# Kernel tuning notes

Measured on AMD Instinct MI355X. Metric: run time of the kernel, lower is better.

The kernel has to match this reference:

```python
import jax, jax.numpy as jnp
import numpy as np

B = 4096
D0, D1 = 256, 64


def setup_inputs() -> dict:
    key = jax.random.key(0)
    k0, k1, k2, k3 = jax.random.split(key, 4)
    return {
        "s0": jax.random.normal(k0, (B, D0), dtype=jnp.float32),
        "s1": jax.random.normal(k1, (B, D1), dtype=jnp.float32),
        "t0": jax.random.normal(k2, (B, D0), dtype=jnp.float32),
        "t1": jax.random.normal(k3, (B, D1), dtype=jnp.float32),
    }


def _gaussian_kernel(source, target):
    # feats: [2B, D]
    feats = jnp.concatenate([source, target], axis=0)
    n = feats.shape[0]
    # pairwise squared distances [2B, 2B] via the Gram-matrix identity
    # (same math as ((x - y) ** 2).sum(-1), avoids the [N, N, D] intermediate)
    sq = jnp.sum(feats * feats, axis=-1)
    dist = sq[:, None] + sq[None, :] - 2.0 * (feats @ feats.T)
    # median-heuristic bandwidth with num_kernels=1: gamma = (n^2 - n) / sum(dist)
    gamma = (n * n - n) / jnp.sum(jax.lax.stop_gradient(dist))
    return jnp.exp(-dist * gamma)


def reference(s0, s1, t0, t1):
    # joint kernel: elementwise product of per-stream Gaussian kernels
    k = _gaussian_kernel(s0, t0) * _gaussian_kernel(s1, t1)
    b = s0.shape[0]
    s2s = k[:b, :b]
    t2t = k[b:, b:]
    s2t = k[:b, b:]
    return jnp.mean(s2s + t2t - 2.0 * s2t)
```

## Files before the change

kernel.cpp:

```cpp
#include <hip/hip_runtime.h>
#include <hip/hip_fp8.h>

#define B_ROWS 4096
#define NTOT   8192
#define D0     256
#define D1     64
#define KDIM   320
#define NSB    128
#define NTILE  64
#define NTRI   2080

typedef __attribute__((ext_vector_type(4))) float f32x4;
typedef __attribute__((ext_vector_type(2))) long long2v;

#define OFF_GAM   0
#define OFF_PQ0   32
#define OFF_PQ1   544
#define OFF_P0    1056
#define OFF_P1    132128
#define OFF_R     164896
#define OFF_BSUM  197664
#define OFF_PHI   214304

__device__ __forceinline__ void load_lds16(const void* g, void* l) {
    __builtin_amdgcn_global_load_lds(
        (const __attribute__((address_space(1))) void*)g,
        (__attribute__((address_space(3))) void*)l, 16, 0, 0);
}

__global__ __launch_bounds__(256) void k_stats(
    const float* __restrict__ s0, const float* __restrict__ s1,
    const float* __restrict__ t0, const float* __restrict__ t1,
    float* __restrict__ part0, float* __restrict__ part1,
    float* __restrict__ pq0, float* __restrict__ pq1) {
    __shared__ float sh0[4][256];
    __shared__ float sh1[4][64];
    __shared__ float shq[4][2];
    int t = threadIdx.x, wv = t >> 6, lane = t & 63;
    int rb = blockIdx.x * 64;
    int c4 = lane * 4;
    int rr = wv;

    f32x4 cs = {0.f, 0.f, 0.f, 0.f};
    float q0 = 0.f;
    #pragma unroll 4
    for (int k = 0; k < 16; ++k) {
        int row = rb + rr + k * 4;
        const float* b0 = (row < B_ROWS) ? s0 + (size_t)row * D0 : t0 + (size_t)(row - B_ROWS) * D0;
        f32x4 v = *(const f32x4*)(b0 + c4);
        cs.x += v.x; cs.y += v.y; cs.z += v.z; cs.w += v.w;
        q0 += v.x * v.x + v.y * v.y + v.z * v.z + v.w * v.w;
    }
    *(f32x4*)&sh0[rr][c4] = cs;

    float cs1 = 0.f, q1 = 0.f;
    #pragma unroll 4
    for (int k = 0; k < 16; ++k) {
        int row = rb + rr + k * 4;
        const float* b1 = (row < B_ROWS) ? s1 + (size_t)row * D1 : t1 + (size_t)(row - B_ROWS) * D1;
        float v = b1[lane];
        cs1 += v; q1 += v * v;
    }
    sh1[rr][lane] = cs1;

    #pragma unroll
    for (int o = 32; o; o >>= 1) { q0 += __shfl_xor(q0, o, 64); q1 += __shfl_xor(q1, o, 64); }
    if (lane == 0) { shq[wv][0] = q0; shq[wv][1] = q1; }
    __syncthreads();

    part0[blockIdx.x * D0 + t] = sh0[0][t] + sh0[1][t] + sh0[2][t] + sh0[3][t];
    if (t < D1) part1[blockIdx.x * D1 + t] = sh1[0][t] + sh1[1][t] + sh1[2][t] + sh1[3][t];
    if (t == 0) {
        pq0[blockIdx.x] = shq[0][0] + shq[1][0] + shq[2][0] + shq[3][0];
        pq1[blockIdx.x] = shq[0][1] + shq[1][1] + shq[2][1] + shq[3][1];
    }
}

__global__ __launch_bounds__(256) void k_gamma(
    const float* __restrict__ pq0, const float* __restrict__ pq1,
    const float* __restrict__ part0, const float* __restrict__ part1,
    float* __restrict__ gam) {
    __shared__ double sh[4][4];
    int t = threadIdx.x, wv = t >> 6, lane = t & 63;

    double a0 = 0.0, a1 = 0.0;
    if (t < NSB) { a0 = (double)pq0[t]; a1 = (double)pq1[t]; }

    double F0t = 0.0;
    for (int b = 0; b < NSB; ++b) F0t += (double)part0[b * D0 + t];
    double nf0 = F0t * F0t;

    double nf1 = 0.0;
    if (t < D1) {
        double F1t = 0.0;
        for (int b = 0; b < NSB; ++b) F1t += (double)part1[b * D1 + t];
        nf1 = F1t * F1t;
    }

    #pragma unroll
    for (int o = 32; o; o >>= 1) {
        a0  += __shfl_xor(a0, o, 64);
        a1  += __shfl_xor(a1, o, 64);
        nf0 += __shfl_xor(nf0, o, 64);
        nf1 += __shfl_xor(nf1, o, 64);
    }
    if (lane == 0) { sh[wv][0] = a0; sh[wv][1] = a1; sh[wv][2] = nf0; sh[wv][3] = nf1; }
    __syncthreads();
    if (t == 0) {
        double b0 = 0, b1 = 0, b2 = 0, b3 = 0;
        for (int w = 0; w < 4; ++w) { b0 += sh[w][0]; b1 += sh[w][1]; b2 += sh[w][2]; b3 += sh[w][3]; }
        double n = (double)NTOT;
        double g0 = (n * n - n) / (2.0 * n * b0 - 2.0 * b2);
        double g1 = (n * n - n) / (2.0 * n * b1 - 2.0 * b3);
        gam[0] = (float)g0; gam[1] = (float)g1;
        gam[2] = (float)sqrt(g0); gam[3] = (float)sqrt(g1);
    }
}

__global__ __launch_bounds__(256) void k_pack(
    const float* __restrict__ s0, const float* __restrict__ s1,
    const float* __restrict__ t0, const float* __restrict__ t1,
    const float* __restrict__ gam, unsigned char* __restrict__ phi,
    float* __restrict__ rvec) {
    int wv = threadIdx.x >> 6, lane = threadIdx.x & 63;
    int row = blockIdx.x * 4 + wv;
    float sg0 = gam[2], sg1 = gam[3];
    const float* b0 = (row < B_ROWS) ? s0 + (size_t)row * D0 : t0 + (size_t)(row - B_ROWS) * D0;
    const float* b1 = (row < B_ROWS) ? s1 + (size_t)row * D1 : t1 + (size_t)(row - B_ROWS) * D1;
    unsigned char* pr = phi + (size_t)row * KDIM;
    f32x4 v = *(const f32x4*)(b0 + lane * 4);
    __hip_fp8_e4m3 q0(v.x * sg0), q1(v.y * sg0), q2(v.z * sg0), q3(v.w * sg0);
    unsigned int word = (unsigned int)q0.__x | ((unsigned int)q1.__x << 8) |
                        ((unsigned int)q2.__x << 16) | ((unsigned int)q3.__x << 24);
    int doff0 = ((lane >> 4) << 6) + (((lane >> 1) & 3) << 4) +
                (((lane >> 3) & 1) << 3) + ((lane & 1) << 2);
    *(unsigned int*)(pr + doff0) = word;
    float f0 = (float)q0, f1 = (float)q1, f2 = (float)q2, f3 = (float)q3;
    float p = f0 * f0 + f1 * f1 + f2 * f2 + f3 * f3;
    __hip_fp8_e4m3 qd(b1[lane] * sg1);
    int doff1 = 256 + (((lane >> 3) & 3) << 4) + (((lane >> 5) & 1) << 3) + (lane & 7);
    pr[doff1] = qd.__x;
    float fd = (float)qd;
    p += fd * fd;
    #pragma unroll
    for (int o = 32; o; o >>= 1) p += __shfl_xor(p, o, 64);
    if (lane == 0) rvec[row] = p;
}

__global__ __launch_bounds__(256, 3) void k_mmd(
    const unsigned char* __restrict__ phi, const float* __restrict__ rvec,
    double* __restrict__ blocksum) {
    int tb = blockIdx.x;
    int I = (int)((129.0f - sqrtf(16641.0f - 8.0f * (float)tb)) * 0.5f);
    while ((129 * I - I * I) / 2 > tb) --I;
    while ((129 * (I + 1) - (I + 1) * (I + 1)) / 2 <= tb) ++I;
    int J = I + (tb - (129 * I - I * I) / 2);

    __shared__ unsigned char As[24576];
    __shared__ unsigned char Bs[24576];
    __shared__ float rIl[128], rJl[128];
    __shared__ float wsum[4];

    int tid = threadIdx.x, wv = tid >> 6, lane = tid & 63;
    int wr = wv >> 1, wc = wv & 1;
    int rgrp = lane >> 4, rlow = lane & 15;
    const int rowA = I * 128, rowB = J * 128;

    if (tid < 128) rIl[tid] = rvec[rowA + tid];
    else           rJl[tid - 128] = rvec[rowB + (tid - 128)];

    f32x4 acc_[4][4] = {};

    #define STAGE(tbase, nt)                                                    \
        _Pragma("unroll")                                                       \
        for (int it = 0; it < (nt) * 2; ++it) {                                 \
            int idx = it * 256 + tid;                                           \
            int tt = idx >> 9, rs = idx & 511;                                  \
            int row = rs >> 2, slot = rs & 3;                                   \
            int rg = slot ^ ((row >> 1) & 3);                                   \
            size_t gcol = ((tbase) + tt) * 64 + rg * 16;                        \
            load_lds16(phi + (size_t)(rowA + row) * KDIM + gcol,                \
                       As + it * 4096 + wv * 1024);                             \
            load_lds16(phi + (size_t)(rowB + row) * KDIM + gcol,                \
                       Bs + it * 4096 + wv * 1024);                             \
        }

    #define COMPUTE(kkbase, nt)                                                 \
        _Pragma("unroll")                                                       \
        for (int tt = 0; tt < (nt); ++tt) {                                     \
            long2v af[4], bf[4];                                                \
            _Pragma("unroll")                                                   \
            for (int m = 0; m < 4; ++m) {                                       \
                int row = wr * 64 + m * 16 + rlow;                              \
                int slot = rgrp ^ ((row >> 1) & 3);                             \
                af[m] = *(const long2v*)&As[tt * 8192 + row * 64 + slot * 16];  \
            }                                                                   \
            _Pragma("unroll")                                                   \
            for (int n = 0; n < 4; ++n) {                                       \
                int col = wc * 64 + n * 16 + rlow;                              \
                int slot = rgrp ^ ((col >> 1) & 3);                             \
                bf[n] = *(const long2v*)&Bs[tt * 8192 + col * 64 + slot * 16];  \
            }                                                                   \
            _Pragma("unroll")                                                   \
            for (int m = 0; m < 4; ++m)                                         \
                _Pragma("unroll")                                               \
                for (int n = 0; n < 4; ++n) {                                   \
                    acc_[m][n] = __builtin_amdgcn_mfma_f32_16x16x32_fp8_fp8(    \
                        af[m][0], bf[n][0], acc_[m][n], 0, 0, 0);               \
                    acc_[m][n] = __builtin_amdgcn_mfma_f32_16x16x32_fp8_fp8(    \
                        af[m][1], bf[n][1], acc_[m][n], 0, 0, 0);               \
                }                                                               \
        }

    STAGE(0, 3);
    __syncthreads();
    COMPUTE(0, 3);
    __syncthreads();
    STAGE(3, 2);
    __syncthreads();
    COMPUTE(6, 2);

    float psum = 0.f;
    #pragma unroll
    for (int m = 0; m < 4; ++m) {
        float ri[4];
        #pragma unroll
        for (int j = 0; j < 4; ++j) ri[j] = rIl[wr * 64 + m * 16 + rgrp * 4 + j];
        #pragma unroll
        for (int n = 0; n < 4; ++n) {
            float rj = rJl[wc * 64 + n * 16 + rlow];
            f32x4 a = acc_[m][n];
            psum += __expf(2.f * a.x - ri[0] - rj);
            psum += __expf(2.f * a.y - ri[1] - rj);
            psum += __expf(2.f * a.z - ri[2] - rj);
            psum += __expf(2.f * a.w - ri[3] - rj);
        }
    }
    #pragma unroll
    for (int o = 32; o; o >>= 1) psum += __shfl_xor(psum, o, 64);
    if (lane == 0) wsum[wv] = psum;
    __syncthreads();
    if (tid == 0) {
        float bs = wsum[0] + wsum[1] + wsum[2] + wsum[3];
        double sgn = ((I < 32) == (J < 32)) ? 1.0 : -1.0;
        double fac = (I == J) ? 1.0 : 2.0;
        blocksum[tb] = sgn * fac * (double)bs;
    }
}

__global__ __launch_bounds__(256) void k_final(
    const double* __restrict__ blocksum, float* __restrict__ out) {
    __shared__ double sh[4];
    int t = threadIdx.x, wv = t >> 6, lane = t & 63;
    double s = 0.0;
    for (int i = t; i < NTRI; i += 256) s += blocksum[i];
    #pragma unroll
    for (int o = 32; o; o >>= 1) s += __shfl_xor(s, o, 64);
    if (lane == 0) sh[wv] = s;
    __syncthreads();
    if (t == 0) {
        double tot = sh[0] + sh[1] + sh[2] + sh[3];
        out[0] = (float)(tot / ((double)B_ROWS * (double)B_ROWS));
    }
}

extern "C" void kernel_launch(void* const* d_in, const int* in_sizes, int n_in,
                              void* d_out, int out_size, void* d_ws, size_t ws_size,
                              hipStream_t stream) {
    const float* s0 = (const float*)d_in[0];
    const float* s1 = (const float*)d_in[1];
    const float* t0 = (const float*)d_in[2];
    const float* t1 = (const float*)d_in[3];
    char* ws = (char*)d_ws;
    float*  gam  = (float*)(ws + OFF_GAM);
    float*  pq0  = (float*)(ws + OFF_PQ0);
    float*  pq1  = (float*)(ws + OFF_PQ1);
    float*  p0   = (float*)(ws + OFF_P0);
    float*  p1   = (float*)(ws + OFF_P1);
    float*  rvec = (float*)(ws + OFF_R);
    double* bsum = (double*)(ws + OFF_BSUM);
    unsigned char* phi = (unsigned char*)(ws + OFF_PHI);

    k_stats<<<NSB, 256, 0, stream>>>(s0, s1, t0, t1, p0, p1, pq0, pq1);
    k_gamma<<<1, 256, 0, stream>>>(pq0, pq1, p0, p1, gam);
    k_pack<<<2048, 256, 0, stream>>>(s0, s1, t0, t1, gam, phi, rvec);
    k_mmd<<<NTRI, 256, 0, stream>>>(phi, rvec, bsum);
    k_final<<<1, 256, 0, stream>>>(bsum, (float*)d_out);
}
```

Before: 49.73 us.

## Make MMD kernel persistent and prefetch next tile during exp epilogue

The MMD kernel now launches 768 persistent blocks, and each one strides over the 2080 triangular tiles. While the exp/reduction epilogue of the current tile runs, the block issues the async LDS loads for the first K-stage of its next tile. MFMA sections are also wrapped in s_setprio raises. The aim is to hide global-to-LDS latency and cut launch/tail overhead. The cost is that work is spread unevenly: 2080 tiles over 768 blocks gives 2 or 3 tiles per block, which can leave a tail imbalance.

```diff
diff --git a/kernel.cpp b/kernel.cpp
--- a/kernel.cpp
+++ b/kernel.cpp
@@ -9,6 +9,7 @@
 #define NSB    128
 #define NTILE  64
 #define NTRI   2080
+#define PERS   768
 
 typedef __attribute__((ext_vector_type(4))) float f32x4;
 typedef __attribute__((ext_vector_type(2))) long long2v;
@@ -150,12 +151,6 @@
 __global__ __launch_bounds__(256, 3) void k_mmd(
     const unsigned char* __restrict__ phi, const float* __restrict__ rvec,
     double* __restrict__ blocksum) {
-    int tb = blockIdx.x;
-    int I = (int)((129.0f - sqrtf(16641.0f - 8.0f * (float)tb)) * 0.5f);
-    while ((129 * I - I * I) / 2 > tb) --I;
-    while ((129 * (I + 1) - (I + 1) * (I + 1)) / 2 <= tb) ++I;
-    int J = I + (tb - (129 * I - I * I) / 2);
-
     __shared__ unsigned char As[24576];
     __shared__ unsigned char Bs[24576];
     __shared__ float rIl[128], rJl[128];
@@ -164,14 +159,14 @@
     int tid = threadIdx.x, wv = tid >> 6, lane = tid & 63;
     int wr = wv >> 1, wc = wv & 1;
     int rgrp = lane >> 4, rlow = lane & 15;
-    const int rowA = I * 128, rowB = J * 128;
-
-    if (tid < 128) rIl[tid] = rvec[rowA + tid];
-    else           rJl[tid - 128] = rvec[rowB + (tid - 128)];
-
-    f32x4 acc_[4][4] = {};
-
-    #define STAGE(tbase, nt)                                                    \
+
+    #define DECODE(tb_, I_, J_)                                                 \
+        I_ = (int)((129.0f - sqrtf(16641.0f - 8.0f * (float)(tb_))) * 0.5f);    \
+        while ((129 * I_ - I_ * I_) / 2 > (tb_)) --I_;                          \
+        while ((129 * (I_ + 1) - (I_ + 1) * (I_ + 1)) / 2 <= (tb_)) ++I_;       \
+        J_ = I_ + ((tb_) - (129 * I_ - I_ * I_) / 2);
+
+    #define STAGE(tbase, nt, ra, rb)                                            \
         _Pragma("unroll")                                                       \
         for (int it = 0; it < (nt) * 2; ++it) {                                 \
             int idx = it * 256 + tid;                                           \
@@ -179,28 +174,29 @@
             int row = rs >> 2, slot = rs & 3;                                   \
             int rg = slot ^ ((row >> 1) & 3);                                   \
             size_t gcol = ((tbase) + tt) * 64 + rg * 16;                        \
-            load_lds16(phi + (size_t)(rowA + row) * KDIM + gcol,                \
+            load_lds16(phi + (size_t)((ra) + row) * KDIM + gcol,                \
                        As + it * 4096 + wv * 1024);                             \
-            load_lds16(phi + (size_t)(rowB + row) * KDIM + gcol,                \
+            load_lds16(phi + (size_t)((rb) + row) * KDIM + gcol,                \
                        Bs + it * 4096 + wv * 1024);                             \
         }
 
-    #define COMPUTE(kkbase, nt)                                                 \
+    #define COMPUTE(nt)                                                         \
         _Pragma("unroll")                                                       \
         for (int tt = 0; tt < (nt); ++tt) {                                     \
             long2v af[4], bf[4];                                                \
             _Pragma("unroll")                                                   \
             for (int m = 0; m < 4; ++m) {                                       \
                 int row = wr * 64 + m * 16 + rlow;                              \
-                int slot = rgrp ^ ((row >> 1) & 3);                             \
-                af[m] = *(const long2v*)&As[tt * 8192 + row * 64 + slot * 16];  \
+                int sl = rgrp ^ ((row >> 1) & 3);                               \
+                af[m] = *(const long2v*)&As[tt * 8192 + row * 64 + sl * 16];    \
             }                                                                   \
             _Pragma("unroll")                                                   \
             for (int n = 0; n < 4; ++n) {                                       \
                 int col = wc * 64 + n * 16 + rlow;                              \
-                int slot = rgrp ^ ((col >> 1) & 3);                             \
-                bf[n] = *(const long2v*)&Bs[tt * 8192 + col * 64 + slot * 16];  \
+                int sl = rgrp ^ ((col >> 1) & 3);                               \
+                bf[n] = *(const long2v*)&Bs[tt * 8192 + col * 64 + sl * 16];    \
             }                                                                   \
+            __builtin_amdgcn_s_setprio(1);                                      \
             _Pragma("unroll")                                                   \
             for (int m = 0; m < 4; ++m)                                         \
                 _Pragma("unroll")                                               \
@@ -210,41 +206,66 @@
                     acc_[m][n] = __builtin_amdgcn_mfma_f32_16x16x32_fp8_fp8(    \
                         af[m][1], bf[n][1], acc_[m][n], 0, 0, 0);               \
                 }                                                               \
-        }
-
-    STAGE(0, 3);
-    __syncthreads();
-    COMPUTE(0, 3);
-    __syncthreads();
-    STAGE(3, 2);
-    __syncthreads();
-    COMPUTE(6, 2);
-
-    float psum = 0.f;
-    #pragma unroll
-    for (int m = 0; m < 4; ++m) {
-        float ri[4];
+            __builtin_amdgcn_s_setprio(0);                                      \
+        }
+
+    int I, J;
+    int tb = blockIdx.x;
+    if (tb >= NTRI) return;
+    DECODE(tb, I, J);
+    int rowA = I * 128, rowB = J * 128;
+    STAGE(0, 3, rowA, rowB);
+
+    while (true) {
+        if (tid < 128) rIl[tid] = rvec[rowA + tid];
+        else           rJl[tid - 128] = rvec[rowB + (tid - 128)];
+        __syncthreads();
+
+        f32x4 acc_[4][4] = {};
+        COMPUTE(3);
+        __syncthreads();
+        STAGE(3, 2, rowA, rowB);
+        __syncthreads();
+        COMPUTE(2);
+        __syncthreads();
+
+        int tbn = tb + PERS;
+        int In, Jn, rowAn = 0, rowBn = 0;
+        if (tbn < NTRI) {
+            DECODE(tbn, In, Jn);
+            rowAn = In * 128; rowBn = Jn * 128;
+            STAGE(0, 3, rowAn, rowBn);
+        }
+
+        float psum = 0.f;
         #pragma unroll
-        for (int j = 0; j < 4; ++j) ri[j] = rIl[wr * 64 + m * 16 + rgrp * 4 + j];
+        for (int m = 0; m < 4; ++m) {
+            float ri[4];
+            #pragma unroll
+            for (int j = 0; j < 4; ++j) ri[j] = rIl[wr * 64 + m * 16 + rgrp * 4 + j];
+            #pragma unroll
+            for (int n = 0; n < 4; ++n) {
+                float rj = rJl[wc * 64 + n * 16 + rlow];
+                f32x4 a = acc_[m][n];
+                psum += __expf(2.f * a.x - ri[0] - rj);
+                psum += __expf(2.f * a.y - ri[1] - rj);
+                psum += __expf(2.f * a.z - ri[2] - rj);
+                psum += __expf(2.f * a.w - ri[3] - rj);
+            }
+        }
         #pragma unroll
-        for (int n = 0; n < 4; ++n) {
-            float rj = rJl[wc * 64 + n * 16 + rlow];
-            f32x4 a = acc_[m][n];
-            psum += __expf(2.f * a.x - ri[0] - rj);
-            psum += __expf(2.f * a.y - ri[1] - rj);
-            psum += __expf(2.f * a.z - ri[2] - rj);
-            psum += __expf(2.f * a.w - ri[3] - rj);
-        }
-    }
-    #pragma unroll
-    for (int o = 32; o; o >>= 1) psum += __shfl_xor(psum, o, 64);
-    if (lane == 0) wsum[wv] = psum;
-    __syncthreads();
-    if (tid == 0) {
-        float bs = wsum[0] + wsum[1] + wsum[2] + wsum[3];
-        double sgn = ((I < 32) == (J < 32)) ? 1.0 : -1.0;
-        double fac = (I == J) ? 1.0 : 2.0;
-        blocksum[tb] = sgn * fac * (double)bs;
+        for (int o = 32; o; o >>= 1) psum += __shfl_xor(psum, o, 64);
+        if (lane == 0) wsum[wv] = psum;
+        __syncthreads();
+        if (tid == 0) {
+            float bs = wsum[0] + wsum[1] + wsum[2] + wsum[3];
+            double sgn = ((I < 32) == (J < 32)) ? 1.0 : -1.0;
+            double fac = (I == J) ? 1.0 : 2.0;
+            blocksum[tb] = sgn * fac * (double)bs;
+        }
+
+        if (tbn >= NTRI) break;
+        tb = tbn; I = In; J = Jn; rowA = rowAn; rowB = rowBn;
     }
 }
 
@@ -284,6 +305,6 @@
     k_stats<<<NSB, 256, 0, stream>>>(s0, s1, t0, t1, p0, p1, pq0, pq1);
     k_gamma<<<1, 256, 0, stream>>>(pq0, pq1, p0, p1, gam);
     k_pack<<<2048, 256, 0, stream>>>(s0, s1, t0, t1, gam, phi, rvec);
-    k_mmd<<<NTRI, 256, 0, stream>>>(phi, rvec, bsum);
+    k_mmd<<<PERS, 256, 0, stream>>>(phi, rvec, bsum);
     k_final<<<1, 256, 0, stream>>>(bsum, (float*)d_out);
 }
```

After: 52.89 us. 1.06x slower.
